# Optimization experiments

Measured on AMD Instinct MI355X. Metric: run time of the kernel, lower is better.

## Reference

```python
import jax, jax.numpy as jnp
import numpy as np

H = 14; W = 14          # feature-map spatial size (forced by .view(...,14,14))
OUT = 3                 # roi_align output_size
GRID = 2                # fixed sampling_ratio (torchvision adaptive default replaced by 2 for jit)
C_IN = 1024; C_MID = 256
NUM_CLS = 27; A = 5; B = 16
EPS = 1e-5


def setup_inputs() -> dict:
    key = jax.random.key(0)
    ks = jax.random.split(key, 16)
    # boxes in fmap coords, guaranteed x2>x1, y2>y1
    x1 = jax.random.uniform(ks[0], (B, A, H * W), minval=0.0, maxval=10.0)
    y1 = jax.random.uniform(ks[1], (B, A, H * W), minval=0.0, maxval=10.0)
    bw = jax.random.uniform(ks[2], (B, A, H * W), minval=1.0, maxval=4.0)
    bh = jax.random.uniform(ks[3], (B, A, H * W), minval=1.0, maxval=4.0)
    boxes = jnp.stack([x1, y1, x1 + bw, y1 + bh], axis=-1)  # [B,A,196,4]
    output_fmap = jax.random.normal(ks[4], (B, C_IN, H, W), dtype=jnp.float32)
    w1 = jax.random.normal(ks[5], (C_IN, C_IN), dtype=jnp.float32) * 0.03
    g1 = jax.random.uniform(ks[6], (C_IN,), minval=0.5, maxval=1.5)
    b1 = jax.random.normal(ks[7], (C_IN,)) * 0.1
    m1 = jax.random.normal(ks[8], (C_IN,)) * 0.1
    v1 = jax.random.uniform(ks[9], (C_IN,), minval=0.5, maxval=1.5)
    w2 = jax.random.normal(ks[10], (C_MID, C_IN), dtype=jnp.float32) * 0.03
    g2 = jax.random.uniform(ks[11], (C_MID,), minval=0.5, maxval=1.5)
    b2 = jax.random.normal(ks[12], (C_MID,)) * 0.1
    m2 = jax.random.normal(ks[13], (C_MID,)) * 0.1
    v2 = jax.random.uniform(ks[14], (C_MID,), minval=0.5, maxval=1.5)
    kfc1, kfc2 = jax.random.split(ks[15])
    wfc = jax.random.normal(kfc1, (NUM_CLS, C_MID * OUT * OUT)) * 0.02
    bfc = jax.random.normal(kfc2, (NUM_CLS,)) * 0.01
    return dict(boxes=boxes, output_fmap=output_fmap, w1=w1, g1=g1, b1=b1, m1=m1,
                v1=v1, w2=w2, g2=g2, b2=b2, m2=m2, v2=v2, wfc=wfc, bfc=bfc)


def _bn(x, g, b, m, v):  # x: [...,C] channels last, eval-mode BN
    return (x - m) * (g * jax.lax.rsqrt(v + EPS)) + b


def _bilinear(fmap, y, x):
    """torchvision roi_align bilinear interp (aligned=False). fmap [H,W,C]; y,x [...]."""
    valid = (y >= -1.0) & (y <= H) & (x >= -1.0) & (x <= W)
    y = jnp.maximum(y, 0.0)
    x = jnp.maximum(x, 0.0)
    yl = jnp.minimum(jnp.floor(y), H - 1).astype(jnp.int32)
    xl = jnp.minimum(jnp.floor(x), W - 1).astype(jnp.int32)
    yh = jnp.minimum(yl + 1, H - 1)
    xh = jnp.minimum(xl + 1, W - 1)
    y = jnp.where(yl == H - 1, jnp.float32(H - 1), y)
    x = jnp.where(xl == W - 1, jnp.float32(W - 1), x)
    ly = y - yl; lx = x - xl; hy = 1.0 - ly; hx = 1.0 - lx
    val = ((hy * hx)[..., None] * fmap[yl, xl]
           + (hy * lx)[..., None] * fmap[yl, xh]
           + (ly * hx)[..., None] * fmap[yh, xl]
           + (ly * lx)[..., None] * fmap[yh, xh])
    return jnp.where(valid[..., None], val, 0.0)


def _roi_align_one(fmap, boxes):
    """fmap [H,W,C], boxes [R,4] (x1,y1,x2,y2) -> [R,OUT,OUT,C]."""
    x1, y1, x2, y2 = (boxes[:, i] for i in range(4))
    rw = jnp.maximum(x2 - x1, 1.0)
    rh = jnp.maximum(y2 - y1, 1.0)
    # sample offsets within roi: bin index + centered sub-sample, in bin units
    offs = jnp.asarray((np.arange(OUT)[:, None] + (np.arange(GRID)[None, :] + 0.5) / GRID)
                       .reshape(-1), dtype=jnp.float32)  # [OUT*GRID]
    ys = (y1[:, None] + offs[None, :] * (rh / OUT)[:, None])[:, :, None]  # [R,6,1]
    xs = (x1[:, None] + offs[None, :] * (rw / OUT)[:, None])[:, None, :]  # [R,1,6]
    y, x = jnp.broadcast_arrays(ys, xs)                                   # [R,6,6]
    vals = _bilinear(fmap, y, x)                                          # [R,6,6,C]
    c = vals.shape[-1]
    return vals.reshape(-1, OUT, GRID, OUT, GRID, c).mean(axis=(2, 4))    # avg pool bins


def reference(boxes, output_fmap, w1, g1, b1, m1, v1, w2, g2, b2, m2, v2, wfc, bfc):
    b_, a_, f_, _ = boxes.shape
    x = jnp.transpose(output_fmap, (0, 2, 3, 1))                 # NHWC
    h = _bn(jnp.einsum('bhwc,oc->bhwo', x, w1), g1, b1, m1, v1)  # 1x1 conv + BN
    fmap = _bn(jnp.einsum('bhwc,oc->bhwo', h, w2), g2, b2, m2, v2)  # [B,H,W,256]
    pooled = jax.vmap(_roi_align_one)(fmap, boxes.reshape(b_, -1, 4))  # [B,R,3,3,C]
    # torch flattens CHW order per roi before the FC
    feats = jnp.transpose(pooled, (0, 1, 4, 2, 3)).reshape(b_, a_ * f_, -1)  # [B,R,2304]
    logits = feats @ wfc.T + bfc                                  # [B,R,num_cls]
    num_cls = wfc.shape[0]
    return logits.reshape(b_, a_ * num_cls, H, W)
```

## Files before the change

kernel.cpp:

```cpp
#include <hip/hip_runtime.h>
#include <hip/hip_bf16.h>
#include <math.h>

#define H_ 14
#define W_ 14
#define HW_ 196
#define CIN_ 1024
#define CMID_ 256
#define NCLS_ 27
#define NB_ 16
#define ROIS_ 980
#define M_ 3136
#define FEAT_ 2304
#define NROI_ (NB_ * ROIS_)
#define NCB_ 256

typedef unsigned short u16;
typedef __attribute__((ext_vector_type(8))) short bf16x8;
typedef __attribute__((ext_vector_type(4))) float f32x4;

__device__ __forceinline__ float bf2f(u16 u) {
    union { unsigned int i; float f; } x; x.i = ((unsigned int)u) << 16; return x.f;
}
__device__ __forceinline__ float bits2f(unsigned int u) {
    union { unsigned int i; float f; } x; x.i = u; return x.f;
}
__device__ __forceinline__ u16 f2bf(float f) {
    __hip_bfloat16 h = __float2bfloat16(f);
    return *reinterpret_cast<u16*>(&h);
}

__global__ __launch_bounds__(256) void k_prep(
    const float* __restrict__ wfc, u16* __restrict__ w_bin,
    const float* __restrict__ w2, const float* __restrict__ g2,
    const float* __restrict__ v2, u16* __restrict__ w2s,
    const float* __restrict__ w1, const float* __restrict__ g1,
    const float* __restrict__ v1, u16* __restrict__ w1ts,
    const float* __restrict__ fmap_in, u16* __restrict__ anhwc)
{
    __shared__ float ld[64][197];
    float (*ld65)[65] = (float(*)[65])&ld[0][0];
    const int bid = blockIdx.x, t = threadIdx.x;
    if (bid < 256) {
        int idx = bid * 256 + t;
        int cb = idx >> 8, c = idx & 255;
        int cls = cb / 9, bin = cb - cls * 9;
        w_bin[idx] = f2bf((cb < 243) ? wfc[cls * FEAT_ + c * 9 + bin] : 0.0f);
        return;
    }
    if (bid < 320) {
        const int b2id = bid - 256;
        const int kt = b2id & 15, ct = b2id >> 4;
        const int rr = t >> 6, cc = t & 63;
        #pragma unroll
        for (int it = 0; it < 16; ++it) {
            int row = it * 4 + rr;
            ld65[row][cc] = w2[(size_t)(ct * 64 + row) * CIN_ + kt * 64 + cc];
        }
        __syncthreads();
        float sc = g2[ct * 64 + cc] * rsqrtf(v2[ct * 64 + cc] + 1e-5f);
        #pragma unroll
        for (int it = 0; it < 16; ++it) {
            int krow = it * 4 + rr;
            w2s[(size_t)(kt * 64 + krow) * CMID_ + ct * 64 + cc] = f2bf(ld65[cc][krow] * sc);
        }
        return;
    }
    if (bid < 576) {
        const int b1id = bid - 320;
        const int ot = b1id & 15, ct = b1id >> 4;
        const int rr = t >> 6, cc = t & 63;
        #pragma unroll
        for (int it = 0; it < 16; ++it) {
            int row = it * 4 + rr;
            ld65[row][cc] = w1[(size_t)(ot * 64 + row) * CIN_ + ct * 64 + cc];
        }
        __syncthreads();
        float sc = g1[ot * 64 + cc] * rsqrtf(v1[ot * 64 + cc] + 1e-5f);
        #pragma unroll
        for (int it = 0; it < 16; ++it) {
            int crow = it * 4 + rr;
            w1ts[(size_t)(ct * 64 + crow) * CIN_ + ot * 64 + cc] = f2bf(ld65[cc][crow] * sc);
        }
        return;
    }
    const int bn = bid - 576;
    const int b = bn >> 4, c0 = (bn & 15) << 6;
    const float* src = fmap_in + ((size_t)b * CIN_ + c0) * HW_;
    #pragma unroll
    for (int it = 0; it < 49; ++it) {
        int idx = it * 256 + t;
        int ci = idx / 196;
        int hw = idx - ci * 196;
        ld[ci][hw] = src[idx];
    }
    __syncthreads();
    u16* dst = anhwc + (size_t)b * HW_ * CIN_ + c0;
    #pragma unroll
    for (int it = 0; it < 49; ++it) {
        int idx = it * 256 + t;
        int hw = idx >> 6, ci = idx & 63;
        dst[(size_t)hw * CIN_ + ci] = f2bf(ld[ci][hw]);
    }
}

__global__ __launch_bounds__(256) void k_cfc(
    const u16* __restrict__ w_bin, const u16* __restrict__ wG,
    const float* __restrict__ g1, const float* __restrict__ b1,
    const float* __restrict__ m1, const float* __restrict__ v1,
    const float* __restrict__ g2, const float* __restrict__ b2,
    const float* __restrict__ m2, const float* __restrict__ v2,
    const float* __restrict__ bfc, float* __restrict__ cfc)
{
    __shared__ float ps[4];
    const int cls = blockIdx.x, t = threadIdx.x;
    float bi2 = b2[t] - m2[t] * (g2[t] * rsqrtf(v2[t] + 1e-5f));
    float s = 0.0f;
    #pragma unroll
    for (int bin = 0; bin < 9; ++bin)
        s += bf2f(w_bin[(cls * 9 + bin) * 256 + t]) * bi2;
    #pragma unroll
    for (int j = 0; j < 4; ++j) {
        int o = t + 256 * j;
        float bi1 = b1[o] - m1[o] * (g1[o] * rsqrtf(v1[o] + 1e-5f));
        #pragma unroll
        for (int bin = 0; bin < 9; ++bin)
            s += bf2f(wG[(size_t)(cls * 9 + bin) * CIN_ + o]) * bi1;
    }
    #pragma unroll
    for (int o = 32; o > 0; o >>= 1) s += __shfl_xor(s, o, 64);
    if ((t & 63) == 0) ps[t >> 6] = s;
    __syncthreads();
    if (t == 0) cfc[cls] = bfc[cls] + ps[0] + ps[1] + ps[2] + ps[3];
}

__global__ __launch_bounds__(512) void k_gemm_sk(
    const u16* __restrict__ A, const u16* __restrict__ Bw, u16* __restrict__ outp,
    int N, int K)
{
    __shared__ u16 As[2][64][72];
    __shared__ u16 Bs[2][64][72];
    __shared__ float red[4096];
    const int row0 = blockIdx.y * 64, col0 = blockIdx.x * 64;
    const int t = threadIdx.x, kw = t >> 8, tt = t & 255;
    const int wave = tt >> 6, lane = tt & 63;
    const int wr = (wave >> 1) * 32, wc = (wave & 1) * 32;
    const int fr = lane & 15, fk = (lane >> 4) * 8;
    const int sr = tt >> 2, sk = (tt & 3) * 16;
    const int Kh = K >> 1;
    const int nkt = Kh >> 6;
    f32x4 acc[2][2] = {};
    const u16* Ap = A + (size_t)(row0 + sr) * K + kw * Kh + sk;
    const u16* Bp = Bw + (size_t)(col0 + sr) * K + kw * Kh + sk;
    uint4 a0 = *reinterpret_cast<const uint4*>(Ap);
    uint4 a1 = *reinterpret_cast<const uint4*>(Ap + 8);
    uint4 b0 = *reinterpret_cast<const uint4*>(Bp);
    uint4 b1 = *reinterpret_cast<const uint4*>(Bp + 8);
    for (int kt = 0; kt < nkt; ++kt) {
        *reinterpret_cast<uint4*>(&As[kw][sr][sk]) = a0;
        *reinterpret_cast<uint4*>(&As[kw][sr][sk + 8]) = a1;
        *reinterpret_cast<uint4*>(&Bs[kw][sr][sk]) = b0;
        *reinterpret_cast<uint4*>(&Bs[kw][sr][sk + 8]) = b1;
        __syncthreads();
        if (kt < nkt - 1) {
            const int k0 = (kt + 1) * 64;
            a0 = *reinterpret_cast<const uint4*>(Ap + k0);
            a1 = *reinterpret_cast<const uint4*>(Ap + k0 + 8);
            b0 = *reinterpret_cast<const uint4*>(Bp + k0);
            b1 = *reinterpret_cast<const uint4*>(Bp + k0 + 8);
        }
        #pragma unroll
        for (int kk = 0; kk < 2; ++kk) {
            const int ko = fk + kk * 32;
            bf16x8 af0 = *reinterpret_cast<bf16x8*>(&As[kw][wr + fr][ko]);
            bf16x8 af1 = *reinterpret_cast<bf16x8*>(&As[kw][wr + 16 + fr][ko]);
            bf16x8 bf0 = *reinterpret_cast<bf16x8*>(&Bs[kw][wc + fr][ko]);
            bf16x8 bf1 = *reinterpret_cast<bf16x8*>(&Bs[kw][wc + 16 + fr][ko]);
            acc[0][0] = __builtin_amdgcn_mfma_f32_16x16x32_bf16(af0, bf0, acc[0][0], 0, 0, 0);
            acc[0][1] = __builtin_amdgcn_mfma_f32_16x16x32_bf16(af0, bf1, acc[0][1], 0, 0, 0);
            acc[1][0] = __builtin_amdgcn_mfma_f32_16x16x32_bf16(af1, bf0, acc[1][0], 0, 0, 0);
            acc[1][1] = __builtin_amdgcn_mfma_f32_16x16x32_bf16(af1, bf1, acc[1][1], 0, 0, 0);
        }
        __syncthreads();
    }
    if (kw == 1) {
        #pragma unroll
        for (int mi = 0; mi < 2; ++mi)
            #pragma unroll
            for (int ni = 0; ni < 2; ++ni)
                #pragma unroll
                for (int rgi = 0; rgi < 4; ++rgi)
                    red[wave * 1024 + lane * 16 + (mi * 2 + ni) * 4 + rgi] = acc[mi][ni][rgi];
    }
    __syncthreads();
    if (kw == 0) {
        #pragma unroll
        for (int mi = 0; mi < 2; ++mi) {
            #pragma unroll
            for (int ni = 0; ni < 2; ++ni) {
                int col = col0 + wc + ni * 16 + fr;
                #pragma unroll
                for (int rgi = 0; rgi < 4; ++rgi) {
                    int row = row0 + wr + mi * 16 + (lane >> 4) * 4 + rgi;
                    float s = acc[mi][ni][rgi]
                            + red[wave * 1024 + lane * 16 + (mi * 2 + ni) * 4 + rgi];
                    outp[(size_t)row * N + col] = f2bf(s);
                }
            }
        }
    }
}

__global__ __launch_bounds__(256) void k_roi_logits(
    const float* __restrict__ boxes, const u16* __restrict__ G,
    const float* __restrict__ cfc, float* __restrict__ out)
{
    __shared__ float sred[4][260];
    const int t = threadIdx.x, w = t >> 6, lane = t & 63;
    const int r = blockIdx.x * 4 + w;
    const int b = r / ROIS_;
    const float* bxp = boxes + (size_t)r * 4;
    float x1 = bxp[0], y1 = bxp[1];
    float rw = fmaxf(bxp[2] - x1, 1.0f), rh = fmaxf(bxp[3] - y1, 1.0f);
    float sx = rw * (1.0f / 3.0f), sy = rh * (1.0f / 3.0f);
    const float OFFS[6] = {0.25f, 0.75f, 1.25f, 1.75f, 2.25f, 2.75f};

    int xl[6], xh[6], yl[6], yh[6];
    float lx[6], hx[6], ly[6], hy[6];
    #pragma unroll
    for (int i = 0; i < 6; ++i) {
        float xx = fmaxf(x1 + OFFS[i] * sx, 0.0f);
        xl[i] = min((int)xx, 13); xh[i] = min(xl[i] + 1, 13);
        float xv = (xl[i] == 13) ? 13.0f : xx;
        lx[i] = xv - (float)xl[i]; hx[i] = 1.0f - lx[i];
        float yy = fmaxf(y1 + OFFS[i] * sy, 0.0f);
        yl[i] = min((int)yy, 13); yh[i] = min(yl[i] + 1, 13);
        float yv = (yl[i] == 13) ? 13.0f : yy;
        ly[i] = yv - (float)yl[i]; hy[i] = 1.0f - ly[i];
    }
    const int xc0 = min(xl[0], 8), yr0 = min(yl[0], 8);

    float WX[3][6], WY[3][6];
    #pragma unroll
    for (int bi = 0; bi < 3; ++bi)
        #pragma unroll
        for (int c = 0; c < 6; ++c) { WX[bi][c] = 0.0f; WY[bi][c] = 0.0f; }
    #pragma unroll
    for (int i = 0; i < 6; ++i) {
        const int bi = i >> 1;
        #pragma unroll
        for (int c = 0; c < 6; ++c) {
            WX[bi][c] += (xl[i] - xc0 == c ? hx[i] : 0.0f)
                       + (xh[i] - xc0 == c ? lx[i] : 0.0f);
            WY[bi][c] += (yl[i] - yr0 == c ? hy[i] : 0.0f)
                       + (yh[i] - yr0 == c ? ly[i] : 0.0f);
        }
    }

    int bxj[4], byj[4];
    #pragma unroll
    for (int j = 0; j < 4; ++j) {
        int cb = lane * 4 + j;
        int cls = cb / 9;
        int bin = cb - cls * 9;
        bxj[j] = bin % 3; byj[j] = bin / 3;
    }
    f32x4 wx4[6], wy4[6];
    #pragma unroll
    for (int q = 0; q < 6; ++q) {
        #pragma unroll
        for (int j = 0; j < 4; ++j) {
            wx4[q][j] = (bxj[j] == 0) ? WX[0][q] : ((bxj[j] == 1) ? WX[1][q] : WX[2][q]);
            wy4[q][j] = (byj[j] == 0) ? WY[0][q] : ((byj[j] == 1) ? WY[1][q] : WY[2][q]);
        }
    }

    const u16* base = G + ((size_t)b * HW_ + yr0 * 14 + xc0) * NCB_ + lane * 4;
    f32x4 acc = {};
    #pragma unroll
    for (int rr = 0; rr < 6; ++rr) {
        const u16* rp = base + rr * (14 * NCB_);
        f32x4 tmp = {};
        #pragma unroll
        for (int cc = 0; cc < 6; ++cc) {
            uint2 gu = *reinterpret_cast<const uint2*>(rp + cc * NCB_);
            f32x4 g;
            g[0] = bits2f(gu.x << 16); g[1] = bits2f(gu.x & 0xFFFF0000u);
            g[2] = bits2f(gu.y << 16); g[3] = bits2f(gu.y & 0xFFFF0000u);
            tmp += g * wx4[cc];
        }
        acc += tmp * wy4[rr];
    }
    acc *= 0.25f;
    #pragma unroll
    for (int j = 0; j < 4; ++j) sred[w][lane * 4 + j] = acc[j];
    __syncthreads();
    if (lane < NCLS_) {
        float s = cfc[lane];
        #pragma unroll
        for (int bin = 0; bin < 9; ++bin) s += sred[w][lane * 9 + bin];
        out[(size_t)r * NCLS_ + lane] = s;
    }
}

extern "C" void kernel_launch(void* const* d_in, const int* in_sizes, int n_in,
                              void* d_out, int out_size, void* d_ws, size_t ws_size,
                              hipStream_t stream) {
    const float* boxes   = (const float*)d_in[0];
    const float* fmap_in = (const float*)d_in[1];
    const float* w1 = (const float*)d_in[2];
    const float* g1 = (const float*)d_in[3];
    const float* b1 = (const float*)d_in[4];
    const float* m1 = (const float*)d_in[5];
    const float* v1 = (const float*)d_in[6];
    const float* w2 = (const float*)d_in[7];
    const float* g2 = (const float*)d_in[8];
    const float* b2 = (const float*)d_in[9];
    const float* m2 = (const float*)d_in[10];
    const float* v2 = (const float*)d_in[11];
    const float* wfc = (const float*)d_in[12];
    const float* bfc = (const float*)d_in[13];

    char* ws = (char*)d_ws;
    u16*   Anhwc = (u16*)(ws + 0);
    u16*   G16   = (u16*)(ws + 6422528);
    u16*   w_bin = (u16*)(ws + 8028160);
    u16*   w2s   = (u16*)(ws + 8159232);
    u16*   w1ts  = (u16*)(ws + 8683520);
    u16*   wG    = (u16*)(ws + 10780672);
    u16*   Wtot  = (u16*)(ws + 11304960);
    float* cfc   = (float*)(ws + 11829248);

    hipLaunchKernelGGL(k_prep, dim3(832), dim3(256), 0, stream,
                       wfc, w_bin, w2, g2, v2, w2s, w1, g1, v1, w1ts, fmap_in, Anhwc);
    hipLaunchKernelGGL(k_gemm_sk, dim3(CIN_ / 64, NCB_ / 64), dim3(512), 0, stream,
                       w_bin, w2s, wG, CIN_, CMID_);
    hipLaunchKernelGGL(k_gemm_sk, dim3(CIN_ / 64, NCB_ / 64), dim3(512), 0, stream,
                       wG, w1ts, Wtot, CIN_, CIN_);
    hipLaunchKernelGGL(k_cfc, dim3(NCLS_), dim3(256), 0, stream,
                       w_bin, wG, g1, b1, m1, v1, g2, b2, m2, v2, bfc, cfc);
    hipLaunchKernelGGL(k_gemm_sk, dim3(NCB_ / 64, M_ / 64), dim3(512), 0, stream,
                       Anhwc, Wtot, G16, NCB_, CIN_);
    hipLaunchKernelGGL(k_roi_logits, dim3(NROI_ / 4), dim3(256), 0, stream,
                       boxes, G16, cfc, (float*)d_out);
}
```

Before: 66.22 us.

## Fold cfc bias into GEMM launch and precompute ROI bilinear weights in prep

Removes the separate cfc kernel launch by running its blocks as extra blocks of the second weight GEMM, which is templated with a 1D grid. ROI bilinear weight tables and base pixel offsets are now computed per ROI in extra blocks of the prep kernel and stored to workspace. The ROI logits kernel then loads these instead of recomputing them in every wave. This trades one fewer launch and less per-wave ALU for an extra global write and read of 40 floats per ROI.

Result: faster. 58.82 us (-11.2%).

```diff
diff --git a/kernel.cpp b/kernel.cpp
--- a/kernel.cpp
+++ b/kernel.cpp
@@ -36,7 +36,8 @@
     const float* __restrict__ v2, u16* __restrict__ w2s,
     const float* __restrict__ w1, const float* __restrict__ g1,
     const float* __restrict__ v1, u16* __restrict__ w1ts,
-    const float* __restrict__ fmap_in, u16* __restrict__ anhwc)
+    const float* __restrict__ fmap_in, u16* __restrict__ anhwc,
+    const float* __restrict__ boxes, float* __restrict__ rw_out)
 {
     __shared__ float ld[64][197];
     float (*ld65)[65] = (float(*)[65])&ld[0][0];
@@ -84,27 +85,76 @@
         }
         return;
     }
-    const int bn = bid - 576;
-    const int b = bn >> 4, c0 = (bn & 15) << 6;
-    const float* src = fmap_in + ((size_t)b * CIN_ + c0) * HW_;
-    #pragma unroll
-    for (int it = 0; it < 49; ++it) {
-        int idx = it * 256 + t;
-        int ci = idx / 196;
-        int hw = idx - ci * 196;
-        ld[ci][hw] = src[idx];
-    }
-    __syncthreads();
-    u16* dst = anhwc + (size_t)b * HW_ * CIN_ + c0;
-    #pragma unroll
-    for (int it = 0; it < 49; ++it) {
-        int idx = it * 256 + t;
-        int hw = idx >> 6, ci = idx & 63;
-        dst[(size_t)hw * CIN_ + ci] = f2bf(ld[ci][hw]);
-    }
-}
-
-__global__ __launch_bounds__(256) void k_cfc(
+    if (bid < 832) {
+        const int bn = bid - 576;
+        const int b = bn >> 4, c0 = (bn & 15) << 6;
+        const float* src = fmap_in + ((size_t)b * CIN_ + c0) * HW_;
+        #pragma unroll
+        for (int it = 0; it < 49; ++it) {
+            int idx = it * 256 + t;
+            int ci = idx / 196;
+            int hw = idx - ci * 196;
+            ld[ci][hw] = src[idx];
+        }
+        __syncthreads();
+        u16* dst = anhwc + (size_t)b * HW_ * CIN_ + c0;
+        #pragma unroll
+        for (int it = 0; it < 49; ++it) {
+            int idx = it * 256 + t;
+            int hw = idx >> 6, ci = idx & 63;
+            dst[(size_t)hw * CIN_ + ci] = f2bf(ld[ci][hw]);
+        }
+        return;
+    }
+    const int r = (bid - 832) * 256 + t;
+    if (r >= NROI_) return;
+    const float* bxp = boxes + (size_t)r * 4;
+    float x1 = bxp[0], y1 = bxp[1];
+    float rwd = fmaxf(bxp[2] - x1, 1.0f), rhd = fmaxf(bxp[3] - y1, 1.0f);
+    float sx = rwd * (1.0f / 3.0f), sy = rhd * (1.0f / 3.0f);
+    const float OFFS[6] = {0.25f, 0.75f, 1.25f, 1.75f, 2.25f, 2.75f};
+    int xl[6], xh[6], yl[6], yh[6];
+    float lx[6], hx[6], ly[6], hy[6];
+    #pragma unroll
+    for (int i = 0; i < 6; ++i) {
+        float xx = fmaxf(x1 + OFFS[i] * sx, 0.0f);
+        xl[i] = min((int)xx, 13); xh[i] = min(xl[i] + 1, 13);
+        float xv = (xl[i] == 13) ? 13.0f : xx;
+        lx[i] = xv - (float)xl[i]; hx[i] = 1.0f - lx[i];
+        float yy = fmaxf(y1 + OFFS[i] * sy, 0.0f);
+        yl[i] = min((int)yy, 13); yh[i] = min(yl[i] + 1, 13);
+        float yv = (yl[i] == 13) ? 13.0f : yy;
+        ly[i] = yv - (float)yl[i]; hy[i] = 1.0f - ly[i];
+    }
+    const int xc0 = min(xl[0], 8), yr0 = min(yl[0], 8);
+    float WX[3][6], WY[3][6];
+    #pragma unroll
+    for (int bi = 0; bi < 3; ++bi)
+        #pragma unroll
+        for (int c = 0; c < 6; ++c) { WX[bi][c] = 0.0f; WY[bi][c] = 0.0f; }
+    #pragma unroll
+    for (int i = 0; i < 6; ++i) {
+        const int bi = i >> 1;
+        #pragma unroll
+        for (int c = 0; c < 6; ++c) {
+            WX[bi][c] += (xl[i] - xc0 == c ? hx[i] : 0.0f)
+                       + (xh[i] - xc0 == c ? lx[i] : 0.0f);
+            WY[bi][c] += (yl[i] - yr0 == c ? hy[i] : 0.0f)
+                       + (yh[i] - yr0 == c ? ly[i] : 0.0f);
+        }
+    }
+    float* ro = rw_out + (size_t)r * 40;
+    #pragma unroll
+    for (int bi = 0; bi < 3; ++bi)
+        #pragma unroll
+        for (int c = 0; c < 6; ++c) { ro[bi * 6 + c] = WX[bi][c]; ro[18 + bi * 6 + c] = WY[bi][c]; }
+    ro[36] = (float)(yr0 * 14 + xc0);
+}
+
+template<bool WITH_CFC>
+__global__ __launch_bounds__(512) void k_gemm_sk(
+    const u16* __restrict__ A, const u16* __restrict__ Bw, u16* __restrict__ outp,
+    int N, int K, int nct,
     const u16* __restrict__ w_bin, const u16* __restrict__ wG,
     const float* __restrict__ g1, const float* __restrict__ b1,
     const float* __restrict__ m1, const float* __restrict__ v1,
@@ -112,36 +162,37 @@
     const float* __restrict__ m2, const float* __restrict__ v2,
     const float* __restrict__ bfc, float* __restrict__ cfc)
 {
-    __shared__ float ps[4];
-    const int cls = blockIdx.x, t = threadIdx.x;
-    float bi2 = b2[t] - m2[t] * (g2[t] * rsqrtf(v2[t] + 1e-5f));
-    float s = 0.0f;
-    #pragma unroll
-    for (int bin = 0; bin < 9; ++bin)
-        s += bf2f(w_bin[(cls * 9 + bin) * 256 + t]) * bi2;
-    #pragma unroll
-    for (int j = 0; j < 4; ++j) {
-        int o = t + 256 * j;
-        float bi1 = b1[o] - m1[o] * (g1[o] * rsqrtf(v1[o] + 1e-5f));
-        #pragma unroll
-        for (int bin = 0; bin < 9; ++bin)
-            s += bf2f(wG[(size_t)(cls * 9 + bin) * CIN_ + o]) * bi1;
-    }
-    #pragma unroll
-    for (int o = 32; o > 0; o >>= 1) s += __shfl_xor(s, o, 64);
-    if ((t & 63) == 0) ps[t >> 6] = s;
-    __syncthreads();
-    if (t == 0) cfc[cls] = bfc[cls] + ps[0] + ps[1] + ps[2] + ps[3];
-}
-
-__global__ __launch_bounds__(512) void k_gemm_sk(
-    const u16* __restrict__ A, const u16* __restrict__ Bw, u16* __restrict__ outp,
-    int N, int K)
-{
     __shared__ u16 As[2][64][72];
     __shared__ u16 Bs[2][64][72];
     __shared__ float red[4096];
-    const int row0 = blockIdx.y * 64, col0 = blockIdx.x * 64;
+    const int bid = blockIdx.x;
+    if (WITH_CFC && bid >= nct) {
+        __shared__ float ps[4];
+        const int cls = bid - nct, t = threadIdx.x;
+        if (t < 256) {
+            float bi2 = b2[t] - m2[t] * (g2[t] * rsqrtf(v2[t] + 1e-5f));
+            float s = 0.0f;
+            #pragma unroll
+            for (int bin = 0; bin < 9; ++bin)
+                s += bf2f(w_bin[(cls * 9 + bin) * 256 + t]) * bi2;
+            #pragma unroll
+            for (int j = 0; j < 4; ++j) {
+                int o = t + 256 * j;
+                float bi1 = b1[o] - m1[o] * (g1[o] * rsqrtf(v1[o] + 1e-5f));
+                #pragma unroll
+                for (int bin = 0; bin < 9; ++bin)
+                    s += bf2f(wG[(size_t)(cls * 9 + bin) * CIN_ + o]) * bi1;
+            }
+            #pragma unroll
+            for (int o = 32; o > 0; o >>= 1) s += __shfl_xor(s, o, 64);
+            if ((t & 63) == 0) ps[t >> 6] = s;
+        }
+        __syncthreads();
+        if (threadIdx.x == 0) cfc[cls] = bfc[cls] + ps[0] + ps[1] + ps[2] + ps[3];
+        return;
+    }
+    const int colt = bid % (N >> 6), rowt = bid / (N >> 6);
+    const int row0 = rowt * 64, col0 = colt * 64;
     const int t = threadIdx.x, kw = t >> 8, tt = t & 255;
     const int wave = tt >> 6, lane = tt & 63;
     const int wr = (wave >> 1) * 32, wc = (wave & 1) * 32;
@@ -152,22 +203,22 @@
     f32x4 acc[2][2] = {};
     const u16* Ap = A + (size_t)(row0 + sr) * K + kw * Kh + sk;
     const u16* Bp = Bw + (size_t)(col0 + sr) * K + kw * Kh + sk;
-    uint4 a0 = *reinterpret_cast<const uint4*>(Ap);
-    uint4 a1 = *reinterpret_cast<const uint4*>(Ap + 8);
-    uint4 b0 = *reinterpret_cast<const uint4*>(Bp);
-    uint4 b1 = *reinterpret_cast<const uint4*>(Bp + 8);
+    uint4 pa0 = *reinterpret_cast<const uint4*>(Ap);
+    uint4 pa1 = *reinterpret_cast<const uint4*>(Ap + 8);
+    uint4 pb0 = *reinterpret_cast<const uint4*>(Bp);
+    uint4 pb1 = *reinterpret_cast<const uint4*>(Bp + 8);
     for (int kt = 0; kt < nkt; ++kt) {
-        *reinterpret_cast<uint4*>(&As[kw][sr][sk]) = a0;
-        *reinterpret_cast<uint4*>(&As[kw][sr][sk + 8]) = a1;
-        *reinterpret_cast<uint4*>(&Bs[kw][sr][sk]) = b0;
-        *reinterpret_cast<uint4*>(&Bs[kw][sr][sk + 8]) = b1;
+        *reinterpret_cast<uint4*>(&As[kw][sr][sk]) = pa0;
+        *reinterpret_cast<uint4*>(&As[kw][sr][sk + 8]) = pa1;
+        *reinterpret_cast<uint4*>(&Bs[kw][sr][sk]) = pb0;
+        *reinterpret_cast<uint4*>(&Bs[kw][sr][sk + 8]) = pb1;
         __syncthreads();
         if (kt < nkt - 1) {
             const int k0 = (kt + 1) * 64;
-            a0 = *reinterpret_cast<const uint4*>(Ap + k0);
-            a1 = *reinterpret_cast<const uint4*>(Ap + k0 + 8);
-            b0 = *reinterpret_cast<const uint4*>(Bp + k0);
-            b1 = *reinterpret_cast<const uint4*>(Bp + k0 + 8);
+            pa0 = *reinterpret_cast<const uint4*>(Ap + k0);
+            pa1 = *reinterpret_cast<const uint4*>(Ap + k0 + 8);
+            pb0 = *reinterpret_cast<const uint4*>(Bp + k0);
+            pb1 = *reinterpret_cast<const uint4*>(Bp + k0 + 8);
         }
         #pragma unroll
         for (int kk = 0; kk < 2; ++kk) {
@@ -212,50 +263,26 @@
 }
 
 __global__ __launch_bounds__(256) void k_roi_logits(
-    const float* __restrict__ boxes, const u16* __restrict__ G,
+    const float* __restrict__ rw, const u16* __restrict__ G,
     const float* __restrict__ cfc, float* __restrict__ out)
 {
     __shared__ float sred[4][260];
     const int t = threadIdx.x, w = t >> 6, lane = t & 63;
     const int r = blockIdx.x * 4 + w;
     const int b = r / ROIS_;
-    const float* bxp = boxes + (size_t)r * 4;
-    float x1 = bxp[0], y1 = bxp[1];
-    float rw = fmaxf(bxp[2] - x1, 1.0f), rh = fmaxf(bxp[3] - y1, 1.0f);
-    float sx = rw * (1.0f / 3.0f), sy = rh * (1.0f / 3.0f);
-    const float OFFS[6] = {0.25f, 0.75f, 1.25f, 1.75f, 2.25f, 2.75f};
-
-    int xl[6], xh[6], yl[6], yh[6];
-    float lx[6], hx[6], ly[6], hy[6];
-    #pragma unroll
-    for (int i = 0; i < 6; ++i) {
-        float xx = fmaxf(x1 + OFFS[i] * sx, 0.0f);
-        xl[i] = min((int)xx, 13); xh[i] = min(xl[i] + 1, 13);
-        float xv = (xl[i] == 13) ? 13.0f : xx;
-        lx[i] = xv - (float)xl[i]; hx[i] = 1.0f - lx[i];
-        float yy = fmaxf(y1 + OFFS[i] * sy, 0.0f);
-        yl[i] = min((int)yy, 13); yh[i] = min(yl[i] + 1, 13);
-        float yv = (yl[i] == 13) ? 13.0f : yy;
-        ly[i] = yv - (float)yl[i]; hy[i] = 1.0f - ly[i];
-    }
-    const int xc0 = min(xl[0], 8), yr0 = min(yl[0], 8);
-
+    const float* rwp = rw + (size_t)r * 40;
     float WX[3][6], WY[3][6];
     #pragma unroll
-    for (int bi = 0; bi < 3; ++bi)
-        #pragma unroll
-        for (int c = 0; c < 6; ++c) { WX[bi][c] = 0.0f; WY[bi][c] = 0.0f; }
-    #pragma unroll
-    for (int i = 0; i < 6; ++i) {
-        const int bi = i >> 1;
-        #pragma unroll
-        for (int c = 0; c < 6; ++c) {
-            WX[bi][c] += (xl[i] - xc0 == c ? hx[i] : 0.0f)
-                       + (xh[i] - xc0 == c ? lx[i] : 0.0f);
-            WY[bi][c] += (yl[i] - yr0 == c ? hy[i] : 0.0f)
-                       + (yh[i] - yr0 == c ? ly[i] : 0.0f);
-        }
-    }
+    for (int q = 0; q < 9; ++q) {
+        f32x4 v = *reinterpret_cast<const f32x4*>(rwp + q * 4);
+        #pragma unroll
+        for (int j = 0; j < 4; ++j) {
+            int idx = q * 4 + j;
+            if (idx < 18) WX[idx / 6][idx % 6] = v[j];
+            else          WY[(idx - 18) / 6][(idx - 18) % 6] = v[j];
+        }
+    }
+    const int basepix = (int)rwp[36];
 
     int bxj[4], byj[4];
     #pragma unroll
@@ -275,7 +302,7 @@
         }
     }
 
-    const u16* base = G + ((size_t)b * HW_ + yr0 * 14 + xc0) * NCB_ + lane * 4;
+    const u16* base = G + ((size_t)b * HW_ + basepix) * NCB_ + lane * 4;
     f32x4 acc = {};
     #pragma unroll
     for (int rr = 0; rr < 6; ++rr) {
@@ -330,17 +357,22 @@
     u16*   wG    = (u16*)(ws + 10780672);
     u16*   Wtot  = (u16*)(ws + 11304960);
     float* cfc   = (float*)(ws + 11829248);
-
-    hipLaunchKernelGGL(k_prep, dim3(832), dim3(256), 0, stream,
-                       wfc, w_bin, w2, g2, v2, w2s, w1, g1, v1, w1ts, fmap_in, Anhwc);
-    hipLaunchKernelGGL(k_gemm_sk, dim3(CIN_ / 64, NCB_ / 64), dim3(512), 0, stream,
-                       w_bin, w2s, wG, CIN_, CMID_);
-    hipLaunchKernelGGL(k_gemm_sk, dim3(CIN_ / 64, NCB_ / 64), dim3(512), 0, stream,
-                       wG, w1ts, Wtot, CIN_, CIN_);
-    hipLaunchKernelGGL(k_cfc, dim3(NCLS_), dim3(256), 0, stream,
+    float* rw    = (float*)(ws + 11829376);
+
+    hipLaunchKernelGGL(k_prep, dim3(832 + 62), dim3(256), 0, stream,
+                       wfc, w_bin, w2, g2, v2, w2s, w1, g1, v1, w1ts, fmap_in, Anhwc,
+                       boxes, rw);
+    hipLaunchKernelGGL((k_gemm_sk<false>), dim3(64), dim3(512), 0, stream,
+                       w_bin, w2s, wG, CIN_, CMID_, 64,
+                       nullptr, nullptr, nullptr, nullptr, nullptr, nullptr,
+                       nullptr, nullptr, nullptr, nullptr, nullptr, nullptr);
+    hipLaunchKernelGGL((k_gemm_sk<true>), dim3(64 + NCLS_), dim3(512), 0, stream,
+                       wG, w1ts, Wtot, CIN_, CIN_, 64,
                        w_bin, wG, g1, b1, m1, v1, g2, b2, m2, v2, bfc, cfc);
-    hipLaunchKernelGGL(k_gemm_sk, dim3(NCB_ / 64, M_ / 64), dim3(512), 0, stream,
-                       Anhwc, Wtot, G16, NCB_, CIN_);
+    hipLaunchKernelGGL((k_gemm_sk<false>), dim3(4 * 49), dim3(512), 0, stream,
+                       Anhwc, Wtot, G16, NCB_, CIN_, 196,
+                       nullptr, nullptr, nullptr, nullptr, nullptr, nullptr,
+                       nullptr, nullptr, nullptr, nullptr, nullptr, nullptr);
     hipLaunchKernelGGL(k_roi_logits, dim3(NROI_ / 4), dim3(256), 0, stream,
-                       boxes, G16, cfc, (float*)d_out);
-}
+                       rw, G16, cfc, (float*)d_out);
+}
```
